# Optimization experiments

Measured on AMD Instinct MI355X. Metric: run time of the kernel, lower is better.

Reference implementation:

```python
import jax, jax.numpy as jnp
import numpy as np

B, N, IN_F, OUT_F, H = 4, 2048, 256, 256, 8
NH = OUT_F // H  # 32
SLOPE = 0.2
NEG_INF = -9e15


def setup_inputs() -> dict:
    key = jax.random.key(0)
    k1, k2, k3, k4 = jax.random.split(key, 4)
    h = jax.random.normal(k1, (B, N, IN_F), jnp.float32)
    adj = jax.random.randint(k2, (B, N, N), 0, 2).astype(jnp.int32)
    # xavier_uniform with gain 1.414
    gw = 1.414 * np.sqrt(6.0 / (IN_F + H * NH))
    W = jax.random.uniform(k3, (IN_F, H * NH), jnp.float32, -gw, gw)
    ga = 1.414 * np.sqrt(6.0 / (2 * NH + 1))
    a = jax.random.uniform(k4, (2 * NH, 1), jnp.float32, -ga, ga)
    return {"h": h, "adj": adj, "W": W, "a": a}


def reference(h, adj, W, a):
    Wh = h @ W                              # [B, N, H*NH]
    # Faithful to torch .view: raw memory reinterpretation, not a transpose.
    Wh = Wh.reshape(B, H, N, NH)            # [B, H, N, NH]
    Wh1 = Wh @ a[:NH]                       # [B, H, N, 1]
    Wh2 = Wh @ a[NH:]                       # [B, H, N, 1]
    e = Wh1 + jnp.swapaxes(Wh2, 2, 3)       # [B, H, N, N] additive scores
    e = jnp.where(e >= 0, e, SLOPE * e)     # leaky relu
    e = jnp.where(adj[:, None] > 0, e, NEG_INF)
    attn = jax.nn.softmax(e, axis=-1)       # [B, H, N, N]
    h_prime = attn @ Wh                     # [B, H, N, NH]
    h_prime = h_prime.reshape(B, N, OUT_F)  # raw reshape, matches torch .view
    return jax.nn.elu(h_prime)
```

## Files before the change

kernel.cpp:

```cpp
#include <hip/hip_runtime.h>
#include <hip/hip_bf16.h>

#define B_    4
#define N_    2048
#define INF_  256
#define OUTF_ 256
#define H_    8
#define NH_   32
#define BH_   (B_ * H_)
#define ROWS_ (B_ * N_)
#define VSZ_  (N_ * NH_)

typedef float  f32x4 __attribute__((ext_vector_type(4)));
typedef short  s16x8 __attribute__((ext_vector_type(8)));

__global__ __launch_bounds__(256) void gemm_wh(const float* __restrict__ A,
                                               const float* __restrict__ Wm,
                                               float* __restrict__ C) {
    __shared__ float As[16][68];
    __shared__ float Bs[16][68];
    const int tid = threadIdx.x;
    const int bm = blockIdx.x * 64;
    const int bn = blockIdx.y * 64;
    const int tm = (tid >> 4) << 2;
    const int tn = (tid & 15) << 2;
    const int ar = tid >> 2, ac = (tid & 3) << 2;
    const int br = tid >> 4, bc = (tid & 15) << 2;
    float acc[4][4] = {};

    for (int k0 = 0; k0 < 256; k0 += 16) {
        float4 av = *(const float4*)(A + (size_t)(bm + ar) * 256 + k0 + ac);
        float4 bv = *(const float4*)(Wm + (size_t)(k0 + br) * 256 + bn + bc);
        As[ac + 0][ar] = av.x;
        As[ac + 1][ar] = av.y;
        As[ac + 2][ar] = av.z;
        As[ac + 3][ar] = av.w;
        *(float4*)&Bs[br][bc] = bv;
        __syncthreads();
#pragma unroll
        for (int kk = 0; kk < 16; ++kk) {
            float a4[4], b4[4];
            *(float4*)a4 = *(const float4*)&As[kk][tm];
            *(float4*)b4 = *(const float4*)&Bs[kk][tn];
#pragma unroll
            for (int i = 0; i < 4; ++i)
#pragma unroll
                for (int j = 0; j < 4; ++j)
                    acc[i][j] = fmaf(a4[i], b4[j], acc[i][j]);
        }
        __syncthreads();
    }
#pragma unroll
    for (int i = 0; i < 4; ++i)
        *(float4*)(C + (size_t)(bm + tm + i) * 256 + bn + tn) = *(float4*)acc[i];
}

__global__ __launch_bounds__(256) void st_kernel(const float* __restrict__ Wh,
                                                 const float* __restrict__ a,
                                                 float* __restrict__ s,
                                                 float* __restrict__ t) {
    const int row = blockIdx.x * 256 + threadIdx.x;
    const float* v = Wh + (size_t)row * NH_;
    float s_ = 0.f, t_ = 0.f;
#pragma unroll
    for (int k = 0; k < NH_; k += 4) {
        float4 vv = *(const float4*)(v + k);
        float4 a1 = *(const float4*)(a + k);
        float4 a2 = *(const float4*)(a + NH_ + k);
        s_ += vv.x * a1.x + vv.y * a1.y + vv.z * a1.z + vv.w * a1.w;
        t_ += vv.x * a2.x + vv.y * a2.y + vv.z * a2.z + vv.w * a2.w;
    }
    s[row] = s_;
    t[row] = t_;
}

__global__ __launch_bounds__(256) void vconv(const float* __restrict__ Wh,
                                             short* __restrict__ Vb) {
    const int t = blockIdx.x * 256 + threadIdx.x;
    const int lane = t & 63;
    const int nt   = (t >> 6) & 1;
    const int jt   = (t >> 7) & 63;
    const int bh   = t >> 13;
    const float* src = Wh + (size_t)bh * VSZ_ +
                       (size_t)(jt * 32 + (lane >> 4) * 8) * NH_ +
                       nt * 16 + (lane & 15);
    s16x8 v;
#pragma unroll
    for (int i = 0; i < 8; ++i) {
        unsigned u = __float_as_uint(src[(size_t)i * NH_]);
        v[i] = (short)((u + 0x7fffu + ((u >> 16) & 1u)) >> 16);
    }
    *(s16x8*)(Vb + (size_t)t * 8) = v;
}

__global__ __launch_bounds__(256) void bitpack(const int* __restrict__ adj,
                                               unsigned int* __restrict__ adjw) {
    const int idx = blockIdx.x * 256 + threadIdx.x;
    const int4* p = (const int4*)(adj + (size_t)idx * 32);
    unsigned int w = 0;
#pragma unroll
    for (int q = 0; q < 8; ++q) {
        int4 v = p[q];
        w |= (v.x != 0 ? 1u : 0u) << (q * 4 + 0);
        w |= (v.y != 0 ? 1u : 0u) << (q * 4 + 1);
        w |= (v.z != 0 ? 1u : 0u) << (q * 4 + 2);
        w |= (v.w != 0 ? 1u : 0u) << (q * 4 + 3);
    }
    adjw[idx] = w;
}

__global__ __launch_bounds__(256) void attn_kernel(const short* __restrict__ Vb,
                                                   const float* __restrict__ s,
                                                   const float* __restrict__ t,
                                                   const unsigned int* __restrict__ adjw,
                                                   float* __restrict__ out) {
    const int bh = blockIdx.y;
    const int b  = bh >> 3;
    const int i0 = blockIdx.x * 64;
    const int tid = threadIdx.x;
    const int wv = tid >> 6;
    const int l  = tid & 63;
    const int lr = l & 15;
    const int lg = l >> 4;

    __shared__ int   adjL[64][68];
    __shared__ float ts[2048];

    {
        const int4* ab = (const int4*)(adjw + (size_t)(b * N_ + i0) * 64);
#pragma unroll
        for (int k = 0; k < 4; ++k) {
            int idx4 = tid + k * 256;
            int4 v = ab[idx4];
            *(int4*)&adjL[idx4 >> 4][(idx4 << 2) & 63] = v;
        }
    }
    {
        const float4* tsrc = (const float4*)(t + (size_t)bh * N_);
        float4 v0 = tsrc[tid];
        float4 v1 = tsrc[tid + 256];
        *(float4*)&ts[tid * 4] = v0;
        *(float4*)&ts[1024 + tid * 4] = v1;
    }
    const float sreg = s[(size_t)bh * N_ + i0 + wv * 16 + lr];
    __syncthreads();

    const s16x8* vb = (const s16x8*)(Vb + (size_t)bh * 65536);

    s16x8 nb0 = vb[l];
    s16x8 nb1 = vb[64 + l];
    f32x4 acc0 = {0.f, 0.f, 0.f, 0.f};
    f32x4 acc1 = {0.f, 0.f, 0.f, 0.f};
    float rs0 = 0.f, rs1 = 0.f;

    for (int jt = 0; jt < 64; ++jt) {
        s16x8 b0 = nb0, b1 = nb1;
        if (jt < 63) {
            nb0 = vb[(jt + 1) * 128 + l];
            nb1 = vb[(jt + 1) * 128 + 64 + l];
        }
        const unsigned wsh = ((unsigned)adjL[wv * 16 + lr][jt]) >> (lg * 8);
        float tv[8];
        *(float4*)&tv[0] = *(const float4*)&ts[jt * 32 + lg * 8];
        *(float4*)&tv[4] = *(const float4*)&ts[jt * 32 + lg * 8 + 4];
        float p[8];
#pragma unroll
        for (int i = 0; i < 8; ++i) {
            float x = sreg + tv[i];
            float e = fmaxf(x, 0.2f * x);
            float pv = __expf(e);
            p[i] = (wsh & (1u << i)) ? pv : 0.f;
        }
        rs0 += p[0] + p[2] + p[4] + p[6];
        rs1 += p[1] + p[3] + p[5] + p[7];
        s16x8 af;
#pragma unroll
        for (int i = 0; i < 8; ++i) {
            unsigned u = __float_as_uint(p[i]);
            af[i] = (short)((u + 0x8000u) >> 16);
        }
        acc0 = __builtin_amdgcn_mfma_f32_16x16x32_bf16(af, b0, acc0, 0, 0, 0);
        acc1 = __builtin_amdgcn_mfma_f32_16x16x32_bf16(af, b1, acc1, 0, 0, 0);
    }

    float rs = rs0 + rs1;
    rs += __shfl_xor(rs, 16);
    rs += __shfl_xor(rs, 32);
    const float inv = 1.0f / rs;

    float* obase = out + (size_t)bh * VSZ_;
#pragma unroll
    for (int r = 0; r < 4; ++r) {
        const int rloc = 4 * lg + r;
        const float ir = __shfl(inv, (l & 48) + rloc);
        const int row = i0 + wv * 16 + rloc;
        float v0 = acc0[r] * ir;
        float v1 = acc1[r] * ir;
        v0 = v0 > 0.f ? v0 : expm1f(v0);
        v1 = v1 > 0.f ? v1 : expm1f(v1);
        obase[(size_t)row * NH_ + lr]      = v0;
        obase[(size_t)row * NH_ + 16 + lr] = v1;
    }
}

extern "C" void kernel_launch(void* const* d_in, const int* in_sizes, int n_in,
                              void* d_out, int out_size, void* d_ws, size_t ws_size,
                              hipStream_t stream) {
    const float* h   = (const float*)d_in[0];
    const int*   adj = (const int*)d_in[1];
    const float* W   = (const float*)d_in[2];
    const float* a   = (const float*)d_in[3];
    float* out = (float*)d_out;

    char* ws = (char*)d_ws;
    float* Wh = (float*)ws;
    char*  p1 = ws + (size_t)ROWS_ * OUTF_ * 4;
    float* s  = (float*)p1;
    float* t  = (float*)(p1 + BH_ * N_ * 4);
    unsigned int* adjw = (unsigned int*)(p1 + 2 * BH_ * N_ * 4);
    short* Vb = (short*)(p1 + 2 * BH_ * N_ * 4 + (size_t)B_ * N_ * 64 * 4);

    gemm_wh<<<dim3(ROWS_ / 64, OUTF_ / 64), 256, 0, stream>>>(h, W, Wh);
    st_kernel<<<(BH_ * N_) / 256, 256, 0, stream>>>(Wh, a, s, t);
    vconv<<<(BH_ * N_ * NH_ / 8) / 256, 256, 0, stream>>>(Wh, Vb);
    bitpack<<<(B_ * N_ * (N_ / 32)) / 256, 256, 0, stream>>>(adj, adjw);
    attn_kernel<<<dim3(N_ / 64, BH_), 256, 0, stream>>>(Vb, s, t, adjw, out);
}
```

Measured before the change: 175.1 us.

## Use bf16 MFMA for projection GEMM and compute row sums via MFMA

Replaces the fp32 SIMT projection GEMM with a conversion kernel that casts h and a pre-fragmented W to bf16, followed by an MFMA-based GEMM. In the attention kernel, masked entries are now set to a large negative before exp rather than zeroed with a select afterward. The softmax row sum comes from an extra MFMA against a ones vector instead of scalar adds and shuffles. This trades an extra launch, workspace traffic and lower GEMM precision for tensor-core throughput, and the row sum is now taken over the bf16-rounded weights.

Result: faster. 166.8 us (-4.7%).

```diff
diff --git a/kernel.cpp b/kernel.cpp
--- a/kernel.cpp
+++ b/kernel.cpp
@@ -14,45 +14,66 @@
 typedef float  f32x4 __attribute__((ext_vector_type(4)));
 typedef short  s16x8 __attribute__((ext_vector_type(8)));
 
-__global__ __launch_bounds__(256) void gemm_wh(const float* __restrict__ A,
-                                               const float* __restrict__ Wm,
-                                               float* __restrict__ C) {
-    __shared__ float As[16][68];
-    __shared__ float Bs[16][68];
+static __device__ __forceinline__ short f2bf(float x) {
+    union { __hip_bfloat16 b; unsigned short u; } cv;
+    cv.b = __float2bfloat16(x);
+    return (short)cv.u;
+}
+
+__global__ __launch_bounds__(256) void hwconv(const float* __restrict__ h,
+                                              const float* __restrict__ W,
+                                              short* __restrict__ hb,
+                                              short* __restrict__ Wf) {
+    const int t = blockIdx.x * 256 + threadIdx.x;
+    if (blockIdx.x < 1024) {
+        const float4* src = (const float4*)(h + (size_t)t * 8);
+        float4 v0 = src[0], v1 = src[1];
+        float vv[8] = {v0.x, v0.y, v0.z, v0.w, v1.x, v1.y, v1.z, v1.w};
+        s16x8 o;
+#pragma unroll
+        for (int i = 0; i < 8; ++i) o[i] = f2bf(vv[i]);
+        *(s16x8*)(hb + (size_t)t * 8) = o;
+    } else {
+        const int u = t - 1024 * 256;
+        const int lane = u & 63, nf = (u >> 6) & 15, kt = u >> 10;
+        const float* src = W + (size_t)(kt * 32 + (lane >> 4) * 8) * 256 +
+                           nf * 16 + (lane & 15);
+        s16x8 o;
+#pragma unroll
+        for (int i = 0; i < 8; ++i) o[i] = f2bf(src[(size_t)i * 256]);
+        *(s16x8*)(Wf + (size_t)u * 8) = o;
+    }
+}
+
+__global__ __launch_bounds__(256) void gemm_mfma(const short* __restrict__ hb,
+                                                 const short* __restrict__ Wf,
+                                                 float* __restrict__ Wh) {
+    const int bm  = blockIdx.x * 64;
+    const int bn4 = blockIdx.y * 4;
     const int tid = threadIdx.x;
-    const int bm = blockIdx.x * 64;
-    const int bn = blockIdx.y * 64;
-    const int tm = (tid >> 4) << 2;
-    const int tn = (tid & 15) << 2;
-    const int ar = tid >> 2, ac = (tid & 3) << 2;
-    const int br = tid >> 4, bc = (tid & 15) << 2;
-    float acc[4][4] = {};
-
-    for (int k0 = 0; k0 < 256; k0 += 16) {
-        float4 av = *(const float4*)(A + (size_t)(bm + ar) * 256 + k0 + ac);
-        float4 bv = *(const float4*)(Wm + (size_t)(k0 + br) * 256 + bn + bc);
-        As[ac + 0][ar] = av.x;
-        As[ac + 1][ar] = av.y;
-        As[ac + 2][ar] = av.z;
-        As[ac + 3][ar] = av.w;
-        *(float4*)&Bs[br][bc] = bv;
-        __syncthreads();
-#pragma unroll
-        for (int kk = 0; kk < 16; ++kk) {
-            float a4[4], b4[4];
-            *(float4*)a4 = *(const float4*)&As[kk][tm];
-            *(float4*)b4 = *(const float4*)&Bs[kk][tn];
-#pragma unroll
-            for (int i = 0; i < 4; ++i)
-#pragma unroll
-                for (int j = 0; j < 4; ++j)
-                    acc[i][j] = fmaf(a4[i], b4[j], acc[i][j]);
-        }
-        __syncthreads();
-    }
-#pragma unroll
-    for (int i = 0; i < 4; ++i)
-        *(float4*)(C + (size_t)(bm + tm + i) * 256 + bn + tn) = *(float4*)acc[i];
+    const int wv = tid >> 6, l = tid & 63;
+    const int lr = l & 15, lg = l >> 4;
+    const int arow = bm + wv * 16 + lr;
+
+    f32x4 acc[4] = {};
+    const s16x8* wf = (const s16x8*)Wf;
+    const s16x8* ha = (const s16x8*)(hb + (size_t)arow * 256 + lg * 8);
+
+#pragma unroll
+    for (int kt = 0; kt < 8; ++kt) {
+        s16x8 a = ha[kt * 4];
+#pragma unroll
+        for (int nf = 0; nf < 4; ++nf) {
+            s16x8 b = wf[(size_t)(kt * 16 + bn4 + nf) * 64 + l];
+            acc[nf] = __builtin_amdgcn_mfma_f32_16x16x32_bf16(a, b, acc[nf], 0, 0, 0);
+        }
+    }
+#pragma unroll
+    for (int nf = 0; nf < 4; ++nf)
+#pragma unroll
+        for (int r = 0; r < 4; ++r)
+            Wh[(size_t)(bm + wv * 16 + 4 * lg + r) * 256 +
+               (size_t)(bn4 + nf) * 16 + lr] = acc[nf][r];
 }
 
 __global__ __launch_bounds__(256) void st_kernel(const float* __restrict__ Wh,
@@ -86,10 +107,7 @@
                        nt * 16 + (lane & 15);
     s16x8 v;
 #pragma unroll
-    for (int i = 0; i < 8; ++i) {
-        unsigned u = __float_as_uint(src[(size_t)i * NH_]);
-        v[i] = (short)((u + 0x7fffu + ((u >> 16) & 1u)) >> 16);
-    }
+    for (int i = 0; i < 8; ++i) v[i] = f2bf(src[(size_t)i * NH_]);
     *(s16x8*)(Vb + (size_t)t * 8) = v;
 }
 
@@ -145,13 +163,17 @@
     const float sreg = s[(size_t)bh * N_ + i0 + wv * 16 + lr];
     __syncthreads();
 
+    s16x8 bOnes;
+#pragma unroll
+    for (int i = 0; i < 8; ++i) bOnes[i] = (lr == 0) ? (short)0x3F80 : (short)0;
+
     const s16x8* vb = (const s16x8*)(Vb + (size_t)bh * 65536);
 
     s16x8 nb0 = vb[l];
     s16x8 nb1 = vb[64 + l];
     f32x4 acc0 = {0.f, 0.f, 0.f, 0.f};
     f32x4 acc1 = {0.f, 0.f, 0.f, 0.f};
-    float rs0 = 0.f, rs1 = 0.f;
+    f32x4 acc2 = {0.f, 0.f, 0.f, 0.f};
 
     for (int jt = 0; jt < 64; ++jt) {
         s16x8 b0 = nb0, b1 = nb1;
@@ -163,36 +185,25 @@
         float tv[8];
         *(float4*)&tv[0] = *(const float4*)&ts[jt * 32 + lg * 8];
         *(float4*)&tv[4] = *(const float4*)&ts[jt * 32 + lg * 8 + 4];
-        float p[8];
+        s16x8 af;
 #pragma unroll
         for (int i = 0; i < 8; ++i) {
             float x = sreg + tv[i];
+            x = (wsh & (1u << i)) ? x : -1.0e6f;
             float e = fmaxf(x, 0.2f * x);
-            float pv = __expf(e);
-            p[i] = (wsh & (1u << i)) ? pv : 0.f;
-        }
-        rs0 += p[0] + p[2] + p[4] + p[6];
-        rs1 += p[1] + p[3] + p[5] + p[7];
-        s16x8 af;
-#pragma unroll
-        for (int i = 0; i < 8; ++i) {
-            unsigned u = __float_as_uint(p[i]);
-            af[i] = (short)((u + 0x8000u) >> 16);
+            af[i] = f2bf(__expf(e));
         }
         acc0 = __builtin_amdgcn_mfma_f32_16x16x32_bf16(af, b0, acc0, 0, 0, 0);
         acc1 = __builtin_amdgcn_mfma_f32_16x16x32_bf16(af, b1, acc1, 0, 0, 0);
-    }
-
-    float rs = rs0 + rs1;
-    rs += __shfl_xor(rs, 16);
-    rs += __shfl_xor(rs, 32);
-    const float inv = 1.0f / rs;
+        acc2 = __builtin_amdgcn_mfma_f32_16x16x32_bf16(af, bOnes, acc2, 0, 0, 0);
+    }
 
     float* obase = out + (size_t)bh * VSZ_;
 #pragma unroll
     for (int r = 0; r < 4; ++r) {
         const int rloc = 4 * lg + r;
-        const float ir = __shfl(inv, (l & 48) + rloc);
+        const float rsum = __shfl(acc2[r], (l & 48));
+        const float ir = 1.0f / rsum;
         const int row = i0 + wv * 16 + rloc;
         float v0 = acc0[r] * ir;
         float v1 = acc1[r] * ir;
@@ -219,8 +230,11 @@
     float* t  = (float*)(p1 + BH_ * N_ * 4);
     unsigned int* adjw = (unsigned int*)(p1 + 2 * BH_ * N_ * 4);
     short* Vb = (short*)(p1 + 2 * BH_ * N_ * 4 + (size_t)B_ * N_ * 64 * 4);
-
-    gemm_wh<<<dim3(ROWS_ / 64, OUTF_ / 64), 256, 0, stream>>>(h, W, Wh);
+    short* hb = (short*)((char*)Vb + (size_t)BH_ * VSZ_ * 2);
+    short* Wf = (short*)((char*)hb + (size_t)ROWS_ * INF_ * 2);
+
+    hwconv<<<1056, 256, 0, stream>>>(h, W, hb, Wf);
+    gemm_mfma<<<dim3(ROWS_ / 64, OUTF_ / 64), 256, 0, stream>>>(hb, Wf, Wh);
     st_kernel<<<(BH_ * N_) / 256, 256, 0, stream>>>(Wh, a, s, t);
     vconv<<<(BH_ * N_ * NH_ / 8) / 256, 256, 0, stream>>>(Wh, Vb);
     bitpack<<<(B_ * N_ * (N_ / 32)) / 256, 256, 0, stream>>>(adj, adjw);
```
